# Optimization experiments

Measured on AMD Instinct MI355X. Metric: run time of the kernel, lower is better.

The kernel has to match this reference:

```python
import jax, jax.numpy as jnp
import numpy as np

NTYPE, NWAVE, NIPSIN = 4, 16, 3
CUTOFF = 5.0
NLOCAL, NALL, NNEIGH = 40000, 48000, 800000
# angular-order index for each of the npara = 1 + 3 + 9 = 13 angular channels
INDEX_PARA = np.concatenate([np.full(3 ** i, i, dtype=np.int32) for i in range(NIPSIN)])


def setup_inputs() -> dict:
    key = jax.random.key(0)
    k0, k1, k2, k3, k4, k5, k6 = jax.random.split(key, 7)
    cart = jax.random.normal(k0, (NALL, 3), dtype=jnp.float32) * 3.0
    i0 = jax.random.randint(k1, (NNEIGH,), 0, NLOCAL, dtype=jnp.int32)
    off = jax.random.randint(k2, (NNEIGH,), 1, NALL, dtype=jnp.int32)
    i1 = (i0 + off) % NALL  # guaranteed != i0 -> no zero distances
    atom_index = jnp.stack([i0, i1], axis=0)
    local_species = jax.random.randint(k3, (NLOCAL,), 0, NTYPE, dtype=jnp.int32)
    neigh_species = jax.random.randint(k4, (NNEIGH,), 0, NTYPE, dtype=jnp.int32)
    rs = jax.random.uniform(k5, (NTYPE, NWAVE), dtype=jnp.float32) * CUTOFF
    inta = 0.5 + jax.random.uniform(k6, (NTYPE, NWAVE), dtype=jnp.float32)
    params = jnp.ones((NTYPE, NWAVE), dtype=jnp.float32)
    return {"cart": cart, "rs": rs, "inta": inta, "params": params,
            "atom_index": atom_index, "local_species": local_species,
            "neigh_species": neigh_species}


def _density(cart, rs, inta, params, atom_index, nlocal, neigh_species):
    # gather neighbor pair coordinates: (2, n, 3)
    sel = cart[atom_index.reshape(-1)].reshape(2, -1, 3)
    dvec = sel[0] - sel[1]                               # (n, 3)
    dist = jnp.linalg.norm(dvec, axis=-1)                # (n,)
    dvec = dvec / dist[:, None]                          # unit vectors
    # cutoff_cosine
    fcut = jnp.square(0.5 * jnp.cos(dist * (np.pi / CUTOFF)) + 0.5)  # (n,)
    # species-gathered gaussian radial basis (vectorized form of per-type masked_scatter loop)
    radial = jnp.exp(-inta[neigh_species] * jnp.square(dist[:, None] - rs[neigh_species]))  # (n, nwave)
    # angular tensor-product channels: concat over orders 0..NIPSIN-1 -> (13, n)
    dvt = dvec.T                                         # (3, n)
    orb = fcut[None, :]                                  # (1, n)
    parts = [orb]
    for _ in range(1, NIPSIN):
        orb = (orb[:, None, :] * dvt[None, :, :]).reshape(-1, orb.shape[1])  # (3^p, n)
        parts.append(orb)
    angular = jnp.concatenate(parts, axis=0)             # (npara, n)
    # outer product per pair: (n, npara, nwave)
    orbital = jnp.einsum('ji,ik->ijk', angular, radial)
    worb = orbital * params[neigh_species][:, None, :]
    # scatter-add over central atoms
    sumw = jnp.zeros((nlocal, angular.shape[0], rs.shape[1]), worb.dtype)
    sumw = sumw.at[atom_index[0]].add(worb)              # (nlocal, npara, nwave)
    # reduce squared channels by angular order
    density = jnp.zeros((nlocal, NIPSIN, rs.shape[1]), worb.dtype)
    density = density.at[:, INDEX_PARA].add(jnp.square(sumw))
    return density.reshape(nlocal, -1)                   # (nlocal, nipsin*nwave)


def reference(cart, rs, inta, params, atom_index, local_species, neigh_species):
    nlocal = local_species.shape[0]
    return _density(cart, rs, inta, params, atom_index, nlocal, neigh_species)
```

## Files before the change

kernel.cpp:

```cpp
#include <hip/hip_runtime.h>
#include <hip/hip_bf16.h>

#define NWAVE 16
#define LOG2CHUNK 14
#define CHUNK (1 << LOG2CHUNK)
#define HIST_WORDS 10240

constexpr float PI_OVER_CUT = 3.14159265358979323846f / 5.0f;


__global__ __launch_bounds__(1024) void chunk_hist_rank(
    const int* __restrict__ idx0, unsigned short* __restrict__ lrank,
    unsigned short* __restrict__ hist16, int nneigh, int halfp)
{
    __shared__ unsigned lds[HIST_WORDS];
    int c = blockIdx.x >> 1;
    int parity = blockIdx.x & 1;
    int t = threadIdx.x;

    int words = halfp >> 1;
    for (int w = t; w < words; w += 1024) lds[w] = 0u;
    __syncthreads();

    int jbeg = c << LOG2CHUNK;
    int jend = jbeg + CHUNK; if (jend > nneigh) jend = nneigh;
    for (int j = jbeg + t; j < jend; j += 1024) {
        int a = idx0[j];
        if ((a & 1) == parity) {
            int bin = a >> 1;
            int word = bin >> 1;
            int shift = (bin & 1) << 4;
            unsigned old = atomicAdd(&lds[word], 1u << shift);
            lrank[j] = (unsigned short)((old >> shift) & 0xffffu);
        }
    }
    __syncthreads();

    unsigned* hrow = (unsigned*)(hist16 + (size_t)blockIdx.x * halfp);
    for (int w = t; w < words; w += 1024) hrow[w] = lds[w];
}


__global__ __launch_bounds__(1024) void count_partial(
    const unsigned short* __restrict__ hist16, unsigned* __restrict__ partials,
    int nlocal, int nc, int halfp)
{
    __shared__ unsigned wsum[16];
    int t = threadIdx.x;
    int lane = t & 63, wid = t >> 6;
    int a = blockIdx.x * 1024 + t;
    unsigned v = 0;
    if (a < nlocal) {
        int parity = a & 1, bin = a >> 1;
        for (int c = 0; c < nc; ++c)
            v += hist16[(size_t)(c * 2 + parity) * halfp + bin];
    }
    #pragma unroll
    for (int o = 32; o >= 1; o >>= 1) v += __shfl_xor(v, o, 64);
    if (lane == 0) wsum[wid] = v;
    __syncthreads();
    if (t == 0) {
        unsigned s = 0;
        #pragma unroll
        for (int i = 0; i < 16; ++i) s += wsum[i];
        partials[blockIdx.x] = s;
    }
}


__global__ __launch_bounds__(1024) void scan_offsets_chunkpre(
    const unsigned short* __restrict__ hist16, const unsigned* __restrict__ partials,
    unsigned* __restrict__ offsets, unsigned short* __restrict__ chunkpreT,
    int nlocal, int nblk, int nc, int halfp, int nlocalp)
{
    __shared__ unsigned wsum[16];
    __shared__ unsigned sOff;
    int t = threadIdx.x;
    int lane = t & 63, wid = t >> 6;
    int a = blockIdx.x * 1024 + t;

    if (wid == 0) {
        unsigned p = (lane < nblk) ? partials[lane] : 0u;
        unsigned incl = p;
        #pragma unroll
        for (int o = 1; o < 64; o <<= 1) {
            unsigned u = __shfl_up(incl, o, 64);
            if (lane >= o) incl += u;
        }
        if (lane == blockIdx.x) sOff = incl - p;
    }

    unsigned v = 0;
    if (a < nlocal) {
        int parity = a & 1, bin = a >> 1;
        for (int c = 0; c < nc; ++c) {
            chunkpreT[(size_t)c * nlocalp + a] = (unsigned short)v;
            v += hist16[(size_t)(c * 2 + parity) * halfp + bin];
        }
    }

    unsigned incl = v;
    #pragma unroll
    for (int o = 1; o < 64; o <<= 1) {
        unsigned u = __shfl_up(incl, o, 64);
        if (lane >= o) incl += u;
    }
    if (lane == 63) wsum[wid] = incl;
    __syncthreads();
    if (t < 16) {
        unsigned u = wsum[t];
        unsigned wincl = u;
        #pragma unroll
        for (int o = 1; o < 16; o <<= 1) {
            unsigned x = __shfl_up(wincl, o, 64);
            if (t >= o) wincl += x;
        }
        wsum[t] = wincl - u;
    }
    __syncthreads();
    if (a < nlocal) {
        unsigned o = sOff + wsum[wid] + (incl - v);
        offsets[a] = o;
        if (a == nlocal - 1) offsets[nlocal] = o + v;
    }
}


__global__ __launch_bounds__(256) void geom_scatter_direct(
    const float* __restrict__ cart, const int* __restrict__ idx0,
    const int* __restrict__ idx1, const int* __restrict__ nspec,
    const unsigned short* __restrict__ lrank, const unsigned* __restrict__ offsets,
    const unsigned short* __restrict__ chunkpreT, float4* __restrict__ srec,
    int nneigh, int nlocalp)
{
    int j = blockIdx.x * blockDim.x + threadIdx.x;
    if (j >= nneigh) return;
    int i0 = idx0[j], i1 = idx1[j], s = nspec[j];
    int c = j >> LOG2CHUNK;
    unsigned p = offsets[i0] + (unsigned)chunkpreT[(size_t)c * nlocalp + i0]
                             + (unsigned)lrank[j];
    float ax = cart[3*i0], ay = cart[3*i0+1], az = cart[3*i0+2];
    float bx = cart[3*i1], by = cart[3*i1+1], bz = cart[3*i1+2];
    float dxv = ax - bx, dyv = ay - by, dzv = az - bz;
    float d2 = dxv*dxv + dyv*dyv + dzv*dzv;
    float rinv = rsqrtf(d2);
    float dist = d2 * rinv;
    unsigned db = (__float_as_uint(dist) & ~3u) | (unsigned)s;
    srec[p] = make_float4(dxv * rinv, dyv * rinv, dzv * rinv, __uint_as_float(db));
}


__global__ __launch_bounds__(256) void density_seq(
    const float* __restrict__ rs, const float* __restrict__ inta,
    const float* __restrict__ params, const unsigned* __restrict__ offsets,
    const float4* __restrict__ srec, float* __restrict__ out,
    int nlocal, int nneigh)
{
    int t = threadIdx.x;
    int lane = t & 63;
    int k = lane & 15, g = lane >> 4;
    int a = blockIdx.x * 4 + (t >> 6);
    if (a >= nlocal) return;

    float rs0 = rs[k],        rs1 = rs[16 + k],     rs2 = rs[32 + k],     rs3 = rs[48 + k];
    float ia0 = inta[k],      ia1 = inta[16 + k],   ia2 = inta[32 + k],   ia3 = inta[48 + k];
    float pp0 = params[k],    pp1 = params[16 + k], pp2 = params[32 + k], pp3 = params[48 + k];

    int beg = (int)offsets[a], end = (int)offsets[a + 1];
    int lim = nneigh - 1;

    float aw = 0.f, axl = 0.f, ayl = 0.f, azl = 0.f;
    float axx = 0.f, ayy = 0.f, azz = 0.f, axy = 0.f, axz = 0.f, ayz = 0.f;

    int p0 = beg + g; if (p0 > lim) p0 = lim;
    float4 rec0 = srec[p0];

    for (int n = beg; n < end; n += 4) {
        int p1 = n + 4 + g; if (p1 > lim) p1 = lim;
        float4 rec1 = srec[p1];

        unsigned u = __float_as_uint(rec0.w);
        float dist = __uint_as_float(u & ~3u);
        bool c1 = (u & 1u) != 0u, c2 = (u & 2u) != 0u;
        float rsel = c2 ? (c1 ? rs3 : rs2) : (c1 ? rs1 : rs0);
        float isel = c2 ? (c1 ? ia3 : ia2) : (c1 ? ia1 : ia0);
        float psel = c2 ? (c1 ? pp3 : pp2) : (c1 ? pp1 : pp0);
        float dd  = dist - rsel;
        float rad = __expf(-isel * dd * dd);
        float fc  = fmaf(0.5f, __cosf(dist * PI_OVER_CUT), 0.5f);
        float w   = rad * fc * fc * psel;
        w = (n + g < end) ? w : 0.f;

        float dx = rec0.x, dy = rec0.y, dz = rec0.z;
        float wx = w * dx, wy = w * dy, wz = w * dz;
        aw  += w;
        axl += wx;  ayl += wy;  azl += wz;
        axx = fmaf(wx, dx, axx);  axy = fmaf(wx, dy, axy);  axz = fmaf(wx, dz, axz);
        ayy = fmaf(wy, dy, ayy);  ayz = fmaf(wy, dz, ayz);  azz = fmaf(wz, dz, azz);

        rec0 = rec1;
    }

    #define RED2(x) x += __shfl_xor(x, 16, 64); x += __shfl_xor(x, 32, 64)
    RED2(aw); RED2(axl); RED2(ayl); RED2(azl);
    RED2(axx); RED2(ayy); RED2(azz); RED2(axy); RED2(axz); RED2(ayz);
    #undef RED2

    if (g == 0) {
        float l0 = aw * aw;
        float l1 = axl*axl + ayl*ayl + azl*azl;
        float l2 = axx*axx + ayy*ayy + azz*azz + 2.f*(axy*axy + axz*axz + ayz*ayz);
        out[a*48 + k]      = l0;
        out[a*48 + 16 + k] = l1;
        out[a*48 + 32 + k] = l2;
    }
}


__global__ void hist_kernel(const int* __restrict__ idx0, unsigned* __restrict__ counts, int nneigh) {
    int j = blockIdx.x * blockDim.x + threadIdx.x;
    if (j < nneigh) atomicAdd(&counts[idx0[j]], 1u);
}

__global__ void scan_kernel_1blk(const unsigned* __restrict__ counts, unsigned* __restrict__ offsets,
                                 unsigned* __restrict__ cursor, int nlocal) {
    __shared__ unsigned part[1024];
    int t = threadIdx.x;
    int ch = (nlocal + 1023) / 1024;
    int base = t * ch;
    unsigned s = 0;
    for (int i = 0; i < ch; ++i) { int id = base + i; if (id < nlocal) s += counts[id]; }
    part[t] = s;
    __syncthreads();
    for (int off = 1; off < 1024; off <<= 1) {
        unsigned v = (t >= off) ? part[t - off] : 0u;
        __syncthreads();
        part[t] += v;
        __syncthreads();
    }
    unsigned run = (t == 0) ? 0u : part[t - 1];
    for (int i = 0; i < ch; ++i) {
        int id = base + i;
        if (id < nlocal) { offsets[id] = run; cursor[id] = run; run += counts[id]; }
    }
    if (t == 1023) offsets[nlocal] = part[1023];
}

__global__ __launch_bounds__(256) void scatter_idx(const int* __restrict__ idx0,
                                                   unsigned* __restrict__ cursor,
                                                   unsigned* __restrict__ sorted, int nneigh) {
    int j = blockIdx.x * blockDim.x + threadIdx.x;
    if (j < nneigh) {
        unsigned p = atomicAdd(&cursor[idx0[j]], 1u);
        sorted[p] = (unsigned)j;
    }
}

__global__ __launch_bounds__(256) void density_kernel(
    const float* __restrict__ cart, const float* __restrict__ rs,
    const float* __restrict__ inta, const float* __restrict__ params,
    const int* __restrict__ idx1, const int* __restrict__ nspec,
    const unsigned* __restrict__ offsets, const unsigned* __restrict__ sorted,
    float* __restrict__ out, int nlocal)
{
    int lane = threadIdx.x & 63;
    int a = blockIdx.x * 4 + (threadIdx.x >> 6);
    if (a >= nlocal) return;
    int k = lane & 15;
    int g = lane >> 4;
    float c0x = cart[3*a], c0y = cart[3*a+1], c0z = cart[3*a+2];
    int a1, b1, a2, b2;
    switch (g) {
      case 0:  a1=0; b1=0; a2=1; b2=1; break;
      case 1:  a1=0; b1=1; a2=1; b2=2; break;
      case 2:  a1=0; b1=2; a2=2; b2=0; break;
      default: a1=1; b1=0; a2=2; b2=1; break;
    }
    float acc0 = 0.f, acc1 = 0.f, acc2 = 0.f, acc3 = 0.f;
    unsigned beg = offsets[a], end = offsets[a + 1];
    for (unsigned n = beg; n < end; ++n) {
        int j  = (int)sorted[n];
        int i1 = idx1[j];
        int s  = nspec[j];
        float dxv = c0x - cart[3*i1];
        float dyv = c0y - cart[3*i1+1];
        float dzv = c0z - cart[3*i1+2];
        float d2   = dxv*dxv + dyv*dyv + dzv*dzv;
        float rinv = rsqrtf(d2);
        float dist = d2 * rinv;
        float dx = dxv * rinv, dy = dyv * rinv, dz = dzv * rinv;
        float fc   = 0.5f * __cosf(dist * PI_OVER_CUT) + 0.5f;
        float fcut = fc * fc;
        float tt   = dist - rs[s*NWAVE + k];
        float rad  = __expf(-inta[s*NWAVE + k] * tt * tt) * params[s*NWAVE + k];
        float f1 = (g == 0) ? fcut : fcut * (g == 1 ? dx : (g == 2 ? dy : dz));
        acc0 = fmaf(f1, rad, acc0);
        float pa1 = (a1 == 0 ? dx : (a1 == 1 ? dy : dz));
        float pb1 = (b1 == 0 ? dx : (b1 == 1 ? dy : dz));
        acc1 = fmaf(fcut * pa1 * pb1, rad, acc1);
        float pa2 = (a2 == 0 ? dx : (a2 == 1 ? dy : dz));
        float pb2 = (b2 == 0 ? dx : (b2 == 1 ? dy : dz));
        acc2 = fmaf(fcut * pa2 * pb2, rad, acc2);
        if (g == 0) acc3 = fmaf(fcut * dz * dz, rad, acc3);
    }
    float l0, l1, l2;
    if (g == 0) { l0 = acc0*acc0; l1 = 0.f;        l2 = acc1*acc1 + acc2*acc2 + acc3*acc3; }
    else        { l0 = 0.f;       l1 = acc0*acc0;  l2 = acc1*acc1 + acc2*acc2; }
    l0 += __shfl_xor(l0, 16, 64); l1 += __shfl_xor(l1, 16, 64); l2 += __shfl_xor(l2, 16, 64);
    l0 += __shfl_xor(l0, 32, 64); l1 += __shfl_xor(l1, 32, 64); l2 += __shfl_xor(l2, 32, 64);
    if (g == 0) {
        out[a*48 + k]      = l0;
        out[a*48 + 16 + k] = l1;
        out[a*48 + 32 + k] = l2;
    }
}


extern "C" void kernel_launch(void* const* d_in, const int* in_sizes, int n_in,
                              void* d_out, int out_size, void* d_ws, size_t ws_size,
                              hipStream_t stream) {
    const float* cart   = (const float*)d_in[0];
    const float* rs     = (const float*)d_in[1];
    const float* inta   = (const float*)d_in[2];
    const float* params = (const float*)d_in[3];
    const int* atom_index    = (const int*)d_in[4];
    const int* neigh_species = (const int*)d_in[6];
    int nlocal = in_sizes[5];
    int nneigh = in_sizes[6];
    const int* idx0 = atom_index;
    const int* idx1 = atom_index + nneigh;

    int tb = 256;
    int nblkN = (nneigh + tb - 1) / tb;
    int nc = (nneigh + CHUNK - 1) >> LOG2CHUNK;
    int halfp = (((nlocal + 1) >> 1) + 63) & ~63;
    int nlocalp = (nlocal + 63) & ~63;
    int nblkB = (nlocal + 1023) / 1024;

    char* ws = (char*)d_ws;
    size_t off = 0;
    auto carve = [&](size_t bytes) -> char* {
        off = (off + 255) & ~(size_t)255;
        char* p = ws + off; off += bytes; return p;
    };
    unsigned* counts        = (unsigned*)carve((size_t)nlocal * 4);
    unsigned* offsets       = (unsigned*)carve(((size_t)nlocal + 1) * 4);
    unsigned* cursor        = (unsigned*)carve((size_t)nlocal * 4);
    unsigned* partials      = (unsigned*)carve(256 * 4);
    float4*   srec          = (float4*)carve((size_t)nneigh * 16);
    unsigned short* lrank   = (unsigned short*)carve((size_t)nneigh * 2);
    unsigned short* hist16  = (unsigned short*)carve((size_t)nc * 2 * halfp * 2);
    unsigned short* chunkpreT = (unsigned short*)carve((size_t)nc * nlocalp * 2);
    size_t need_fast = off;

    bool fast = (ws_size >= need_fast) && (nblkB <= 64) &&
                (halfp <= 2 * HIST_WORDS) && (nc <= 64);

    if (fast) {
        chunk_hist_rank<<<nc * 2, 1024, 0, stream>>>(idx0, lrank, hist16, nneigh, halfp);
        count_partial<<<nblkB, 1024, 0, stream>>>(hist16, partials, nlocal, nc, halfp);
        scan_offsets_chunkpre<<<nblkB, 1024, 0, stream>>>(hist16, partials, offsets,
                                                          chunkpreT, nlocal, nblkB, nc,
                                                          halfp, nlocalp);
        geom_scatter_direct<<<nblkN, tb, 0, stream>>>(cart, idx0, idx1, neigh_species,
                                                      lrank, offsets, chunkpreT, srec,
                                                      nneigh, nlocalp);
        density_seq<<<(nlocal + 3) / 4, 256, 0, stream>>>(rs, inta, params, offsets, srec,
                                                          (float*)d_out, nlocal, nneigh);
    } else {
        unsigned* sorted = (unsigned*)srec;
        hipMemsetAsync(counts, 0, (size_t)nlocal * 4, stream);
        hist_kernel<<<nblkN, tb, 0, stream>>>(idx0, counts, nneigh);
        scan_kernel_1blk<<<1, 1024, 0, stream>>>(counts, offsets, cursor, nlocal);
        scatter_idx<<<nblkN, tb, 0, stream>>>(idx0, cursor, sorted, nneigh);
        density_kernel<<<(nlocal + 3) / 4, 256, 0, stream>>>(cart, rs, inta, params, idx1,
                                                             neigh_species, offsets, sorted,
                                                             (float*)d_out, nlocal);
    }
}
```

Baseline: 80.17 us.

## Use 8-bit chunk histograms with fused partial counts and precomputed cutoff

Replaces the parity-split 16-bit per-chunk histograms with single 8-bit histograms over smaller chunks. The per-block partial sums are folded into the histogram kernel through atomics, which removes the separate count_partial kernel. The geometry scatter now precomputes the cosine cutoff and stores the unit direction as fp16, so the density loop skips the cos evaluation. This relies on per-atom counts per chunk and cumulative prefixes fitting in 8 bits, and it lowers direction precision.

```diff
diff --git a/kernel.cpp b/kernel.cpp
--- a/kernel.cpp
+++ b/kernel.cpp
@@ -1,24 +1,26 @@
 #include <hip/hip_runtime.h>
 #include <hip/hip_bf16.h>
+#include <hip/hip_fp16.h>
 
 #define NWAVE 16
-#define LOG2CHUNK 14
+#define LOG2CHUNK 13
 #define CHUNK (1 << LOG2CHUNK)
-#define HIST_WORDS 10240
+#define HIST8_WORDS 10240
 
 constexpr float PI_OVER_CUT = 3.14159265358979323846f / 5.0f;
 
 
-__global__ __launch_bounds__(1024) void chunk_hist_rank(
-    const int* __restrict__ idx0, unsigned short* __restrict__ lrank,
-    unsigned short* __restrict__ hist16, int nneigh, int halfp)
-{
-    __shared__ unsigned lds[HIST_WORDS];
-    int c = blockIdx.x >> 1;
-    int parity = blockIdx.x & 1;
+__global__ __launch_bounds__(1024) void chunk_hist_rank8(
+    const int* __restrict__ idx0, unsigned char* __restrict__ lrank8,
+    unsigned char* __restrict__ hist8, unsigned* __restrict__ partials,
+    int nneigh, int nlocalp, int nblkB)
+{
+    __shared__ unsigned lds[HIST8_WORDS];
+    int c = blockIdx.x;
     int t = threadIdx.x;
-
-    int words = halfp >> 1;
+    int lane = t & 63, wid = t >> 6;
+    int words = nlocalp >> 2;
+
     for (int w = t; w < words; w += 1024) lds[w] = 0u;
     __syncthreads();
 
@@ -26,52 +28,35 @@
     int jend = jbeg + CHUNK; if (jend > nneigh) jend = nneigh;
     for (int j = jbeg + t; j < jend; j += 1024) {
         int a = idx0[j];
-        if ((a & 1) == parity) {
-            int bin = a >> 1;
-            int word = bin >> 1;
-            int shift = (bin & 1) << 4;
-            unsigned old = atomicAdd(&lds[word], 1u << shift);
-            lrank[j] = (unsigned short)((old >> shift) & 0xffffu);
+        unsigned word = (unsigned)a >> 2;
+        unsigned shift = ((unsigned)a & 3u) << 3;
+        unsigned old = atomicAdd(&lds[word], 1u << shift);
+        lrank8[j] = (unsigned char)((old >> shift) & 0xffu);
+    }
+    __syncthreads();
+
+    unsigned* hrow = (unsigned*)(hist8 + (size_t)c * nlocalp);
+    for (int w = t; w < words; w += 1024) hrow[w] = lds[w];
+
+    for (int grp = wid; grp < nblkB; grp += 16) {
+        int base = grp << 8;
+        int stop = base + 256; if (stop > words) stop = words;
+        unsigned s = 0;
+        for (int w = base + lane; w < stop; w += 64) {
+            unsigned v = lds[w];
+            s += (v & 0xffu) + ((v >> 8) & 0xffu) + ((v >> 16) & 0xffu) + (v >> 24);
         }
-    }
-    __syncthreads();
-
-    unsigned* hrow = (unsigned*)(hist16 + (size_t)blockIdx.x * halfp);
-    for (int w = t; w < words; w += 1024) hrow[w] = lds[w];
-}
-
-
-__global__ __launch_bounds__(1024) void count_partial(
-    const unsigned short* __restrict__ hist16, unsigned* __restrict__ partials,
-    int nlocal, int nc, int halfp)
-{
-    __shared__ unsigned wsum[16];
-    int t = threadIdx.x;
-    int lane = t & 63, wid = t >> 6;
-    int a = blockIdx.x * 1024 + t;
-    unsigned v = 0;
-    if (a < nlocal) {
-        int parity = a & 1, bin = a >> 1;
-        for (int c = 0; c < nc; ++c)
-            v += hist16[(size_t)(c * 2 + parity) * halfp + bin];
-    }
-    #pragma unroll
-    for (int o = 32; o >= 1; o >>= 1) v += __shfl_xor(v, o, 64);
-    if (lane == 0) wsum[wid] = v;
-    __syncthreads();
-    if (t == 0) {
-        unsigned s = 0;
         #pragma unroll
-        for (int i = 0; i < 16; ++i) s += wsum[i];
-        partials[blockIdx.x] = s;
+        for (int o = 32; o >= 1; o >>= 1) s += __shfl_xor(s, o, 64);
+        if (lane == 0 && s) atomicAdd(&partials[grp], s);
     }
 }
 
 
 __global__ __launch_bounds__(1024) void scan_offsets_chunkpre(
-    const unsigned short* __restrict__ hist16, const unsigned* __restrict__ partials,
-    unsigned* __restrict__ offsets, unsigned short* __restrict__ chunkpreT,
-    int nlocal, int nblk, int nc, int halfp, int nlocalp)
+    const unsigned char* __restrict__ hist8, const unsigned* __restrict__ partials,
+    unsigned* __restrict__ offsets, unsigned char* __restrict__ chunkpre8,
+    int nlocal, int nblk, int nc, int nlocalp)
 {
     __shared__ unsigned wsum[16];
     __shared__ unsigned sOff;
@@ -92,10 +77,9 @@
 
     unsigned v = 0;
     if (a < nlocal) {
-        int parity = a & 1, bin = a >> 1;
         for (int c = 0; c < nc; ++c) {
-            chunkpreT[(size_t)c * nlocalp + a] = (unsigned short)v;
-            v += hist16[(size_t)(c * 2 + parity) * halfp + bin];
+            chunkpre8[(size_t)c * nlocalp + a] = (unsigned char)v;
+            v += hist8[(size_t)c * nlocalp + a];
         }
     }
 
@@ -129,31 +113,40 @@
 __global__ __launch_bounds__(256) void geom_scatter_direct(
     const float* __restrict__ cart, const int* __restrict__ idx0,
     const int* __restrict__ idx1, const int* __restrict__ nspec,
-    const unsigned short* __restrict__ lrank, const unsigned* __restrict__ offsets,
-    const unsigned short* __restrict__ chunkpreT, float4* __restrict__ srec,
+    const unsigned char* __restrict__ lrank8, const unsigned* __restrict__ offsets,
+    const unsigned char* __restrict__ chunkpre8, uint4* __restrict__ srec,
     int nneigh, int nlocalp)
 {
     int j = blockIdx.x * blockDim.x + threadIdx.x;
     if (j >= nneigh) return;
     int i0 = idx0[j], i1 = idx1[j], s = nspec[j];
     int c = j >> LOG2CHUNK;
-    unsigned p = offsets[i0] + (unsigned)chunkpreT[(size_t)c * nlocalp + i0]
-                             + (unsigned)lrank[j];
+    unsigned p = offsets[i0] + (unsigned)chunkpre8[(size_t)c * nlocalp + i0]
+                             + (unsigned)lrank8[j];
     float ax = cart[3*i0], ay = cart[3*i0+1], az = cart[3*i0+2];
     float bx = cart[3*i1], by = cart[3*i1+1], bz = cart[3*i1+2];
     float dxv = ax - bx, dyv = ay - by, dzv = az - bz;
     float d2 = dxv*dxv + dyv*dyv + dzv*dzv;
     float rinv = rsqrtf(d2);
     float dist = d2 * rinv;
-    unsigned db = (__float_as_uint(dist) & ~3u) | (unsigned)s;
-    srec[p] = make_float4(dxv * rinv, dyv * rinv, dzv * rinv, __uint_as_float(db));
+    float fc = fmaf(0.5f, __cosf(dist * PI_OVER_CUT), 0.5f);
+    float fcut = fc * fc;
+    unsigned hx = __half_as_ushort(__float2half_rn(dxv * rinv));
+    unsigned hy = __half_as_ushort(__float2half_rn(dyv * rinv));
+    unsigned hz = __half_as_ushort(__float2half_rn(dzv * rinv));
+    uint4 r;
+    r.x = hx | (hy << 16);
+    r.y = hz | ((unsigned)s << 16);
+    r.z = __float_as_uint(dist);
+    r.w = __float_as_uint(fcut);
+    srec[p] = r;
 }
 
 
 __global__ __launch_bounds__(256) void density_seq(
     const float* __restrict__ rs, const float* __restrict__ inta,
     const float* __restrict__ params, const unsigned* __restrict__ offsets,
-    const float4* __restrict__ srec, float* __restrict__ out,
+    const uint4* __restrict__ srec, float* __restrict__ out,
     int nlocal, int nneigh)
 {
     int t = threadIdx.x;
@@ -173,25 +166,28 @@
     float axx = 0.f, ayy = 0.f, azz = 0.f, axy = 0.f, axz = 0.f, ayz = 0.f;
 
     int p0 = beg + g; if (p0 > lim) p0 = lim;
-    float4 rec0 = srec[p0];
+    uint4 rec0 = srec[p0];
 
     for (int n = beg; n < end; n += 4) {
         int p1 = n + 4 + g; if (p1 > lim) p1 = lim;
-        float4 rec1 = srec[p1];
-
-        unsigned u = __float_as_uint(rec0.w);
-        float dist = __uint_as_float(u & ~3u);
-        bool c1 = (u & 1u) != 0u, c2 = (u & 2u) != 0u;
+        uint4 rec1 = srec[p1];
+
+        int s = (int)(rec0.y >> 16);
+        bool c1 = (s & 1) != 0, c2 = (s & 2) != 0;
+        float dist = __uint_as_float(rec0.z);
+        float fcut = __uint_as_float(rec0.w);
         float rsel = c2 ? (c1 ? rs3 : rs2) : (c1 ? rs1 : rs0);
         float isel = c2 ? (c1 ? ia3 : ia2) : (c1 ? ia1 : ia0);
         float psel = c2 ? (c1 ? pp3 : pp2) : (c1 ? pp1 : pp0);
         float dd  = dist - rsel;
         float rad = __expf(-isel * dd * dd);
-        float fc  = fmaf(0.5f, __cosf(dist * PI_OVER_CUT), 0.5f);
-        float w   = rad * fc * fc * psel;
+        float w   = rad * fcut * psel;
         w = (n + g < end) ? w : 0.f;
 
-        float dx = rec0.x, dy = rec0.y, dz = rec0.z;
+        float dx = __half2float(__ushort_as_half((unsigned short)(rec0.x & 0xffffu)));
+        float dy = __half2float(__ushort_as_half((unsigned short)(rec0.x >> 16)));
+        float dz = __half2float(__ushort_as_half((unsigned short)(rec0.y & 0xffffu)));
+
         float wx = w * dx, wy = w * dy, wz = w * dz;
         aw  += w;
         axl += wx;  ayl += wy;  azl += wz;
@@ -333,8 +329,7 @@
     int tb = 256;
     int nblkN = (nneigh + tb - 1) / tb;
     int nc = (nneigh + CHUNK - 1) >> LOG2CHUNK;
-    int halfp = (((nlocal + 1) >> 1) + 63) & ~63;
-    int nlocalp = (nlocal + 63) & ~63;
+    int nlocalp = (nlocal + 255) & ~255;
     int nblkB = (nlocal + 1023) / 1024;
 
     char* ws = (char*)d_ws;
@@ -343,27 +338,28 @@
         off = (off + 255) & ~(size_t)255;
         char* p = ws + off; off += bytes; return p;
     };
-    unsigned* counts        = (unsigned*)carve((size_t)nlocal * 4);
-    unsigned* offsets       = (unsigned*)carve(((size_t)nlocal + 1) * 4);
-    unsigned* cursor        = (unsigned*)carve((size_t)nlocal * 4);
-    unsigned* partials      = (unsigned*)carve(256 * 4);
-    float4*   srec          = (float4*)carve((size_t)nneigh * 16);
-    unsigned short* lrank   = (unsigned short*)carve((size_t)nneigh * 2);
-    unsigned short* hist16  = (unsigned short*)carve((size_t)nc * 2 * halfp * 2);
-    unsigned short* chunkpreT = (unsigned short*)carve((size_t)nc * nlocalp * 2);
-    size_t need_fast = off;
-
-    bool fast = (ws_size >= need_fast) && (nblkB <= 64) &&
-                (halfp <= 2 * HIST_WORDS) && (nc <= 64);
+    unsigned* offsets        = (unsigned*)carve(((size_t)nlocal + 1) * 4);
+    unsigned* partials       = (unsigned*)carve(256 * 4);
+    uint4*    srec           = (uint4*)carve((size_t)nneigh * 16);
+    unsigned char* lrank8    = (unsigned char*)carve((size_t)nneigh);
+    unsigned char* hist8     = (unsigned char*)carve((size_t)nc * nlocalp);
+    unsigned char* chunkpre8 = (unsigned char*)carve((size_t)nc * nlocalp);
+    unsigned* counts         = (unsigned*)carve((size_t)nlocal * 4);
+    unsigned* cursor         = (unsigned*)carve((size_t)nlocal * 4);
+    size_t need = off;
+
+    bool fast = (ws_size >= need) && (nblkB <= 64) &&
+                (nlocalp <= 4 * HIST8_WORDS) && (nc <= 512);
 
     if (fast) {
-        chunk_hist_rank<<<nc * 2, 1024, 0, stream>>>(idx0, lrank, hist16, nneigh, halfp);
-        count_partial<<<nblkB, 1024, 0, stream>>>(hist16, partials, nlocal, nc, halfp);
-        scan_offsets_chunkpre<<<nblkB, 1024, 0, stream>>>(hist16, partials, offsets,
-                                                          chunkpreT, nlocal, nblkB, nc,
-                                                          halfp, nlocalp);
+        hipMemsetAsync(partials, 0, (size_t)nblkB * 4, stream);
+        chunk_hist_rank8<<<nc, 1024, 0, stream>>>(idx0, lrank8, hist8, partials,
+                                                  nneigh, nlocalp, nblkB);
+        scan_offsets_chunkpre<<<nblkB, 1024, 0, stream>>>(hist8, partials, offsets,
+                                                          chunkpre8, nlocal, nblkB, nc,
+                                                          nlocalp);
         geom_scatter_direct<<<nblkN, tb, 0, stream>>>(cart, idx0, idx1, neigh_species,
-                                                      lrank, offsets, chunkpreT, srec,
+                                                      lrank8, offsets, chunkpre8, srec,
                                                       nneigh, nlocalp);
         density_seq<<<(nlocal + 3) / 4, 256, 0, stream>>>(rs, inta, params, offsets, srec,
                                                           (float*)d_out, nlocal, nneigh);
```

Measured after the change: 113.8 us. 1.42x slower.
